# Performance work log

Measured on AMD Instinct MI355X. Metric: run time of the kernel, lower is better.

Reference implementation:

```python
import jax, jax.numpy as jnp
import numpy as np

C = 256
CQK = C // 8  # query/key projection dim


def setup_inputs() -> dict:
    key = jax.random.key(0)
    ks = jax.random.split(key, 8)
    B, H, W = 4, 64, 64
    x = jax.random.normal(ks[0], (B, C, H, W), dtype=jnp.float32)
    # 1x1 Conv1d == per-position linear: weight [out, in], bias [out]
    Wq = jax.random.normal(ks[1], (CQK, C), dtype=jnp.float32) * (1.0 / np.sqrt(C))
    bq = jax.random.normal(ks[2], (CQK,), dtype=jnp.float32) * 0.01
    Wk = jax.random.normal(ks[3], (CQK, C), dtype=jnp.float32) * (1.0 / np.sqrt(C))
    bk = jax.random.normal(ks[4], (CQK,), dtype=jnp.float32) * 0.01
    Wv = jax.random.normal(ks[5], (C, C), dtype=jnp.float32) * (1.0 / np.sqrt(C))
    bv = jax.random.normal(ks[6], (C,), dtype=jnp.float32) * 0.01
    gamma = jax.random.normal(ks[7], (1,), dtype=jnp.float32) * 0.1
    return {"x": x, "Wq": Wq, "bq": bq, "Wk": Wk, "bk": bk,
            "Wv": Wv, "bv": bv, "gamma": gamma}


def reference(x, Wq, bq, Wk, bk, Wv, bv, gamma):
    B, Cc, H, W = x.shape
    xf = x.reshape(B, Cc, H * W)                      # [B, C, N]
    q = jnp.einsum('oc,bcn->bon', Wq, xf) + bq[:, None]   # [B, C/8, N]
    k = jnp.einsum('oc,bcn->bon', Wk, xf) + bk[:, None]   # [B, C/8, N]
    v = jnp.einsum('oc,bcn->bon', Wv, xf) + bv[:, None]   # [B, C,   N]
    # energy = q^T k  (unscaled, SAGAN-style)
    energy = jnp.einsum('bon,bom->bnm', q, k)              # [B, N, N]
    attn = jax.nn.softmax(energy, axis=-1)                 # rows over key dim
    # out = value @ attention^T
    out = jnp.einsum('bcm,bnm->bcn', v, attn)              # [B, C, N]
    out = out.reshape(B, Cc, H, W)
    return gamma * out + x
```

## Files before the change

kernel.cpp:

```cpp
#include <hip/hip_runtime.h>
#include <math.h>
#include <stdint.h>

#define N_POS 4096
#define C_DIM 256
#define CQK_D 32
#define NSPLIT 3

typedef __attribute__((ext_vector_type(8))) short bf16x8;
typedef __attribute__((ext_vector_type(4))) float f32x4;
typedef __attribute__((ext_vector_type(4))) uint32_t u32x4;

__device__ inline uint16_t f2bf(float f){
  uint32_t u = __float_as_uint(f);
  return (uint16_t)((u + 0x7FFFu + ((u>>16)&1u)) >> 16);
}
__device__ inline uint32_t pk2bf(float a, float b){
  return (uint32_t)f2bf(a) | ((uint32_t)f2bf(b)<<16);
}
__device__ inline float bf2f_lo(uint32_t d){ return __uint_as_float(d << 16); }
__device__ inline float bf2f_hi(uint32_t d){ return __uint_as_float(d & 0xFFFF0000u); }

__global__ __launch_bounds__(256) void prep(
    const float* __restrict__ x,
    const float* __restrict__ Wq, const float* __restrict__ bq,
    const float* __restrict__ Wk, const float* __restrict__ bk,
    const float* __restrict__ Wv, const float* __restrict__ bv,
    ushort* __restrict__ xT_bf, ushort* __restrict__ W_bf, float* __restrict__ bias_f)
{
    const int tid = threadIdx.x;
    if (blockIdx.x == 64) {
        const int sub = blockIdx.z * 4 + blockIdx.y;
        const int e0 = sub * 5120;
        for (int e = e0 + tid; e < e0 + 5120; e += 256) {
            const int o = e >> 8, c = e & 255;
            float w;
            if (o < 32)       w = Wq[o*C_DIM + c];
            else if (o < 64)  w = Wk[(o-32)*C_DIM + c];
            else              w = Wv[(o-64)*C_DIM + c];
            W_bf[e] = f2bf(w);
        }
        if (sub == 0) {
            for (int i = tid; i < 320; i += 256)
                bias_f[i] = (i < 32) ? bq[i] : (i < 64) ? bk[i-32] : bv[i-64];
        }
        return;
    }
    __shared__ float t[64][65];
    const int jj = tid & 63;
    const int ig = tid >> 6;
    const int n0 = blockIdx.x * 64;
    const int c0 = blockIdx.y * 64;
    const int b  = blockIdx.z;
    #pragma unroll
    for (int ii = 0; ii < 16; ++ii) {
        const int cl = ii*4 + ig;
        t[cl][jj] = x[((size_t)(b*C_DIM) + c0 + cl)*N_POS + n0 + jj];
    }
    __syncthreads();
    #pragma unroll
    for (int ii = 0; ii < 8; ++ii) {
        const int flat = ii*256 + tid;
        const int nl = flat >> 5;
        const int cp = flat & 31;
        const uint32_t d = pk2bf(t[2*cp][nl], t[2*cp+1][nl]);
        *reinterpret_cast<uint32_t*>(xT_bf + ((size_t)(b*N_POS) + n0 + nl)*C_DIM + c0 + 2*cp) = d;
    }
}

__global__ __launch_bounds__(256, 2) void qkv_gemm(
    const ushort* __restrict__ xT_bf, const ushort* __restrict__ W_bf,
    const float* __restrict__ bias_f,
    ushort* __restrict__ q_bf, ushort* __restrict__ k_bf, ushort* __restrict__ v_bf)
{
    __shared__ ushort xs[64*C_DIM];
    const int tid  = threadIdx.x;
    const int wv   = tid >> 6;
    const int lane = tid & 63;
    const int g    = lane >> 4;
    const int q    = lane & 15;
    const int b    = blockIdx.y;
    const int n0   = blockIdx.x * 64;

    {
        const char* xTb = (const char*)(xT_bf + ((size_t)(b*N_POS) + n0)*C_DIM);
        const int n_l    = (tid*16) >> 9;
        const int inner  = (tid & 31) << 4;
        #pragma unroll
        for (int s = 0; s < 8; ++s) {
            const int n = s*8 + n_l;
            const int src_inner = inner ^ ((n & 7) << 4);
            __builtin_amdgcn_global_load_lds(
                (const __attribute__((address_space(1))) uint32_t*)(xTb + (size_t)n*512 + src_inner),
                (__attribute__((address_space(3))) uint32_t*)((char*)xs + s*4096 + wv*1024),
                16, 0, 0);
        }
    }
    __syncthreads();

    f32x4 zero4 = {0.f,0.f,0.f,0.f};
    f32x4 acc[20];
    #pragma unroll
    for (int i = 0; i < 20; ++i) acc[i] = zero4;

    const char* xrow = (const char*)xs + (wv*16 + q)*512;
    const int sw = (q & 7) << 4;

    #pragma unroll
    for (int kk = 0; kk < 8; ++kk) {
        const bf16x8 xf = *reinterpret_cast<const bf16x8*>(xrow + ((kk*64 + g*16) ^ sw));
        const ushort* wrow = W_bf + q*C_DIM + kk*32 + g*8;
        #pragma unroll
        for (int ot = 0; ot < 20; ++ot) {
            const bf16x8 wf = *reinterpret_cast<const bf16x8*>(wrow + ot*16*C_DIM);
            acc[ot] = __builtin_amdgcn_mfma_f32_16x16x32_bf16(wf, xf, acc[ot], 0, 0, 0);
        }
    }

    const int n = n0 + wv*16 + q;
    #pragma unroll
    for (int ot = 0; ot < 4; ++ot) {
        const int ob = ot*16 + 4*g;
        const float4 bi = *reinterpret_cast<const float4*>(bias_f + ob);
        const uint32_t u0 = pk2bf(acc[ot][0] + bi.x, acc[ot][1] + bi.y);
        const uint32_t u1 = pk2bf(acc[ot][2] + bi.z, acc[ot][3] + bi.w);
        ushort* dst = (ot < 2 ? q_bf : k_bf) + ((size_t)(b*N_POS) + n)*CQK_D + (ob & 31);
        uint2 u; u.x = u0; u.y = u1;
        *reinterpret_cast<uint2*>(dst) = u;
    }
    ushort* vB = v_bf + (size_t)(b*C_DIM)*N_POS + n;
    #pragma unroll
    for (int ot = 4; ot < 20; ++ot) {
        const int ob = ot*16 + 4*g;
        const float4 bi = *reinterpret_cast<const float4*>(bias_f + ob);
        const int c = ob - 64;
        vB[(size_t)(c+0)*N_POS] = f2bf(acc[ot][0] + bi.x);
        vB[(size_t)(c+1)*N_POS] = f2bf(acc[ot][1] + bi.y);
        vB[(size_t)(c+2)*N_POS] = f2bf(acc[ot][2] + bi.z);
        vB[(size_t)(c+3)*N_POS] = f2bf(acc[ot][3] + bi.w);
    }
}

__global__ __launch_bounds__(256, 3) void flash_mfma(
    const ushort* __restrict__ q_bf, const ushort* __restrict__ k_bf,
    const ushort* __restrict__ v_bf, ushort* __restrict__ o_part,
    float2* __restrict__ ml)
{
    __shared__ ushort vt[C_DIM*64];
    __shared__ ushort pt[4*16*64];
    __shared__ float  f_s[64];

    const int tid  = threadIdx.x;
    const int wv   = tid >> 6;
    const int lane = tid & 63;
    const int g    = lane >> 4;
    const int q    = lane & 15;
    const int half = blockIdx.y;
    const int b    = blockIdx.z;
    const int n0   = blockIdx.x * 64;
    const int qrow = n0 + wv*16 + q;
    const int mt0  = (half == 0) ? 0 : 22 + (half-1)*21;
    const int mt1  = mt0 + ((half == 0) ? 22 : 21);

    const ushort* qb = q_bf + (size_t)b*N_POS*CQK_D;
    const ushort* kb = k_bf + (size_t)b*N_POS*CQK_D;
    const ushort* vb = v_bf + (size_t)b*C_DIM*N_POS;

    const bf16x8 qfrag = *reinterpret_cast<const bf16x8*>(qb + (size_t)qrow*CQK_D + g*8);

    f32x4 zero4 = {0.f, 0.f, 0.f, 0.f};
    f32x4 acc[4][4];
    #pragma unroll
    for (int i = 0; i < 4; ++i)
        #pragma unroll
        for (int j = 0; j < 4; ++j) acc[i][j] = zero4;
    float m = -INFINITY, l = 0.f;

    const int st_hi = lane >> 3, st_lo = lane & 7;
    const ushort* vsrc0 = vb + (size_t)(wv*64 + st_hi)*N_POS + st_lo*8;
    char* vdst0 = (char*)vt + (wv*64 + st_hi)*128 + (((st_lo ^ st_hi) & 7) << 4);
    char* ptw   = (char*)pt + wv*2048;
    const int swq = (q & 7) << 4;

    auto loadK = [&](int mtx, bf16x8* kf) {
        const int mm = mtx * 64;
        #pragma unroll
        for (int t = 0; t < 4; ++t)
            kf[t] = *reinterpret_cast<const bf16x8*>(kb + (size_t)(mm + t*16 + q)*CQK_D + g*8);
    };

    auto chunk = [&](int mtx, bf16x8* kfc, bf16x8* kfn, int pfmt) {
        const int m0 = mtx * 64;
        __syncthreads();

        u32x4 vreg[8];
        #pragma unroll
        for (int s = 0; s < 8; ++s)
            vreg[s] = *reinterpret_cast<const u32x4*>(vsrc0 + (size_t)s*8*N_POS + m0);

        f32x4 sv[4];
        #pragma unroll
        for (int t = 0; t < 4; ++t)
            sv[t] = __builtin_amdgcn_mfma_f32_16x16x32_bf16(kfc[t], qfrag, zero4, 0, 0, 0);

        float pmax = sv[0][0];
        #pragma unroll
        for (int t = 0; t < 4; ++t)
            #pragma unroll
            for (int r = 0; r < 4; ++r) pmax = fmaxf(pmax, sv[t][r]);
        pmax = fmaxf(pmax, __shfl_xor(pmax, 16));
        pmax = fmaxf(pmax, __shfl_xor(pmax, 32));
        float f = 1.f;
        if (__any(pmax > m + 8.f)) {
            const float mn = fmaxf(m, pmax);
            f = __expf(m - mn);
            l *= f;
            m = mn;
        }
        if (g == 0) f_s[wv*16 + q] = f;

        uint32_t pk[8];
        float psum = 0.f;
        #pragma unroll
        for (int t = 0; t < 4; ++t) {
            const float p0 = __expf(sv[t][0]-m), p1 = __expf(sv[t][1]-m);
            const float p2 = __expf(sv[t][2]-m), p3 = __expf(sv[t][3]-m);
            psum += (p0+p1)+(p2+p3);
            pk[2*t]   = pk2bf(p0, p1);
            pk[2*t+1] = pk2bf(p2, p3);
        }
        psum += __shfl_xor(psum, 16);
        psum += __shfl_xor(psum, 32);
        l += psum;

        loadK(pfmt, kfn);

        #pragma unroll
        for (int t = 0; t < 4; ++t) {
            const int a = q*128 + ((t*32 + g*8) ^ swq);
            *reinterpret_cast<uint32_t*>(ptw + a)     = pk[2*t];
            *reinterpret_cast<uint32_t*>(ptw + a + 4) = pk[2*t+1];
        }
        #pragma unroll
        for (int s = 0; s < 8; ++s)
            *reinterpret_cast<u32x4*>(vdst0 + s*1024) = vreg[s];

        __syncthreads();

        float f4[4];
        #pragma unroll
        for (int qt = 0; qt < 4; ++qt) f4[qt] = f_s[qt*16 + q];
        const bool anyr = (f4[0]!=1.f) | (f4[1]!=1.f) | (f4[2]!=1.f) | (f4[3]!=1.f);
        if (__any(anyr)) {
            #pragma unroll
            for (int ct = 0; ct < 4; ++ct)
                #pragma unroll
                for (int qt = 0; qt < 4; ++qt) acc[ct][qt] *= f4[qt];
        }

        #pragma unroll
        for (int mm = 0; mm < 2; ++mm) {
            bf16x8 vf[4];
            #pragma unroll
            for (int ct = 0; ct < 4; ++ct)
                vf[ct] = *reinterpret_cast<const bf16x8*>(
                    (char*)vt + (wv*64 + ct*16 + q)*128 + ((mm*64 + g*16) ^ swq));
            #pragma unroll
            for (int qt = 0; qt < 4; ++qt) {
                const bf16x8 pb = *reinterpret_cast<const bf16x8*>(
                    (char*)pt + qt*2048 + q*128 + ((mm*64 + g*16) ^ swq));
                #pragma unroll
                for (int ct = 0; ct < 4; ++ct)
                    acc[ct][qt] = __builtin_amdgcn_mfma_f32_16x16x32_bf16(vf[ct], pb, acc[ct][qt], 0, 0, 0);
            }
        }
    };

    bf16x8 kfA[4], kfB[4];
    loadK(mt0, kfA);
    int mt = mt0;
    for (; mt + 1 < mt1; mt += 2) {
        chunk(mt,   kfA, kfB, mt + 1);
        chunk(mt+1, kfB, kfA, (mt + 2 < mt1) ? mt + 2 : mt1 - 1);
    }
    if (mt < mt1) chunk(mt, kfA, kfB, mt);

    if (g == 0) {
        float2 v; v.x = m; v.y = l;
        ml[(size_t)((half*4 + b)*N_POS) + qrow] = v;
    }

    __syncthreads();
    if (g == 0) f_s[wv*16 + q] = l;
    __syncthreads();
    float invl[4];
    #pragma unroll
    for (int qt = 0; qt < 4; ++qt) invl[qt] = 1.f / f_s[qt*16 + q];

    char* obase = (char*)o_part + ((size_t)((half*4 + b)*N_POS) + n0)*512;
    #pragma unroll
    for (int qt = 0; qt < 4; ++qt) {
        char* orow = obase + (size_t)(qt*16 + q)*512 + (wv*64 + 4*g)*2;
        #pragma unroll
        for (int ct = 0; ct < 4; ++ct) {
            const uint32_t u0 = pk2bf(acc[ct][qt][0]*invl[qt], acc[ct][qt][1]*invl[qt]);
            const uint32_t u1 = pk2bf(acc[ct][qt][2]*invl[qt], acc[ct][qt][3]*invl[qt]);
            uint2 u; u.x = u0; u.y = u1;
            *reinterpret_cast<uint2*>(orow + ct*32) = u;
        }
    }
}

__global__ __launch_bounds__(256) void out_combine(
    const ushort* __restrict__ o_part, const float2* __restrict__ ml,
    const float* __restrict__ x, const float* __restrict__ gamma,
    float* __restrict__ out)
{
    __shared__ float t[64][65];
    __shared__ float w0s[64], w1s[64], w2s[64];
    const int tid = threadIdx.x;
    const int jj = tid & 63;
    const int ig = tid >> 6;
    const int nt = blockIdx.x;
    const int ct = blockIdx.y;
    const int b  = blockIdx.z;
    const int n0 = nt*64, c0 = ct*64;
    const float gm = gamma[0];

    if (tid < 64) {
        const float2 a0 = ml[(size_t)((0*4 + b)*N_POS) + n0 + tid];
        const float2 a1 = ml[(size_t)((1*4 + b)*N_POS) + n0 + tid];
        const float2 a2 = ml[(size_t)((2*4 + b)*N_POS) + n0 + tid];
        const float mm = fmaxf(a0.x, fmaxf(a1.x, a2.x));
        const float e0 = __expf(a0.x - mm) * a0.y;
        const float e1 = __expf(a1.x - mm) * a1.y;
        const float e2 = __expf(a2.x - mm) * a2.y;
        const float inv = 1.f / (e0 + e1 + e2);
        w0s[tid] = e0 * inv;
        w1s[tid] = e1 * inv;
        w2s[tid] = e2 * inv;
    }
    __syncthreads();

    #pragma unroll
    for (int ii = 0; ii < 8; ++ii) {
        const int flat = ii*256 + tid;
        const int nl = flat >> 5;
        const int cp = flat & 31;
        const size_t off = ((size_t)(b*N_POS) + n0 + nl)*C_DIM + c0 + 2*cp;
        const uint32_t d0 = *reinterpret_cast<const uint32_t*>(o_part + off);
        const uint32_t d1 = *reinterpret_cast<const uint32_t*>(o_part + (size_t)4*N_POS*C_DIM + off);
        const uint32_t d2 = *reinterpret_cast<const uint32_t*>(o_part + (size_t)8*N_POS*C_DIM + off);
        const float w0 = w0s[nl], w1 = w1s[nl], w2 = w2s[nl];
        t[nl][2*cp]   = w0*bf2f_lo(d0) + w1*bf2f_lo(d1) + w2*bf2f_lo(d2);
        t[nl][2*cp+1] = w0*bf2f_hi(d0) + w1*bf2f_hi(d1) + w2*bf2f_hi(d2);
    }
    __syncthreads();
    #pragma unroll
    for (int ii = 0; ii < 16; ++ii) {
        const int cl = ii*4 + ig;
        const size_t idx = ((size_t)(b*C_DIM) + c0 + cl)*N_POS + n0 + jj;
        out[idx] = gm * t[jj][cl] + x[idx];
    }
}

extern "C" void kernel_launch(void* const* d_in, const int* in_sizes, int n_in,
                              void* d_out, int out_size, void* d_ws, size_t ws_size,
                              hipStream_t stream)
{
    const float* x     = (const float*)d_in[0];
    const float* Wq    = (const float*)d_in[1];
    const float* bq    = (const float*)d_in[2];
    const float* Wk    = (const float*)d_in[3];
    const float* bk    = (const float*)d_in[4];
    const float* Wv    = (const float*)d_in[5];
    const float* bv    = (const float*)d_in[6];
    const float* gamma = (const float*)d_in[7];

    ushort* o_part = (ushort*)d_ws;
    ushort* xT_bf  = (ushort*)d_ws;
    float2* ml     = (float2*)(o_part + (size_t)NSPLIT*4*N_POS*C_DIM);
    ushort* q_bf   = (ushort*)(ml + (size_t)NSPLIT*4*N_POS);
    ushort* k_bf   = q_bf + (size_t)4*N_POS*CQK_D;
    ushort* v_bf   = k_bf + (size_t)4*N_POS*CQK_D;
    ushort* W_bf   = v_bf + (size_t)4*C_DIM*N_POS;
    float*  bias_f = (float*)(W_bf + 320*C_DIM);
    float* out = (float*)d_out;

    prep<<<dim3(65,4,4), 256, 0, stream>>>(x, Wq, bq, Wk, bk, Wv, bv, xT_bf, W_bf, bias_f);
    qkv_gemm<<<dim3(64,4), 256, 0, stream>>>(xT_bf, W_bf, bias_f, q_bf, k_bf, v_bf);
    flash_mfma<<<dim3(64,NSPLIT,4), 256, 0, stream>>>(q_bf, k_bf, v_bf, o_part, ml);
    out_combine<<<dim3(64,4,4), 256, 0, stream>>>(o_part, ml, x, gamma, out);
}
```

Baseline: 115.2 us.

## Load V fragments directly from global in flash kernel and split QKV GEMM outputs

In the attention kernel, V tiles no longer go through LDS. Each wave loads its V MFMA fragments straight from global memory into registers, and the P tile is double-buffered in LDS so one barrier per chunk can be dropped. The QKV projection GEMM is split across two blocks along the output-channel dimension, which doubles the grid and halves the accumulators per thread for better occupancy and parallelism. The risks are less coalesced V global loads, since each lane now reads 16-byte pieces from separate rows, and the x tile being loaded into LDS twice.

After: 128.1 us. 11.2% more time.

```diff
diff --git a/kernel.cpp b/kernel.cpp
--- a/kernel.cpp
+++ b/kernel.cpp
@@ -79,7 +79,8 @@
     const int lane = tid & 63;
     const int g    = lane >> 4;
     const int q    = lane & 15;
-    const int b    = blockIdx.y;
+    const int y    = blockIdx.y;
+    const int b    = blockIdx.z;
     const int n0   = blockIdx.x * 64;
 
     {
@@ -99,9 +100,9 @@
     __syncthreads();
 
     f32x4 zero4 = {0.f,0.f,0.f,0.f};
-    f32x4 acc[20];
-    #pragma unroll
-    for (int i = 0; i < 20; ++i) acc[i] = zero4;
+    f32x4 acc[10];
+    #pragma unroll
+    for (int i = 0; i < 10; ++i) acc[i] = zero4;
 
     const char* xrow = (const char*)xs + (wv*16 + q)*512;
     const int sw = (q & 7) << 4;
@@ -109,35 +110,34 @@
     #pragma unroll
     for (int kk = 0; kk < 8; ++kk) {
         const bf16x8 xf = *reinterpret_cast<const bf16x8*>(xrow + ((kk*64 + g*16) ^ sw));
-        const ushort* wrow = W_bf + q*C_DIM + kk*32 + g*8;
-        #pragma unroll
-        for (int ot = 0; ot < 20; ++ot) {
-            const bf16x8 wf = *reinterpret_cast<const bf16x8*>(wrow + ot*16*C_DIM);
-            acc[ot] = __builtin_amdgcn_mfma_f32_16x16x32_bf16(wf, xf, acc[ot], 0, 0, 0);
+        const ushort* wrow = W_bf + (y*10*16 + q)*C_DIM + kk*32 + g*8;
+        #pragma unroll
+        for (int i = 0; i < 10; ++i) {
+            const bf16x8 wf = *reinterpret_cast<const bf16x8*>(wrow + i*16*C_DIM);
+            acc[i] = __builtin_amdgcn_mfma_f32_16x16x32_bf16(wf, xf, acc[i], 0, 0, 0);
         }
     }
 
     const int n = n0 + wv*16 + q;
     #pragma unroll
-    for (int ot = 0; ot < 4; ++ot) {
-        const int ob = ot*16 + 4*g;
+    for (int i = 0; i < 10; ++i) {
+        const int got = y*10 + i;
+        const int ob  = got*16 + 4*g;
         const float4 bi = *reinterpret_cast<const float4*>(bias_f + ob);
-        const uint32_t u0 = pk2bf(acc[ot][0] + bi.x, acc[ot][1] + bi.y);
-        const uint32_t u1 = pk2bf(acc[ot][2] + bi.z, acc[ot][3] + bi.w);
-        ushort* dst = (ot < 2 ? q_bf : k_bf) + ((size_t)(b*N_POS) + n)*CQK_D + (ob & 31);
-        uint2 u; u.x = u0; u.y = u1;
-        *reinterpret_cast<uint2*>(dst) = u;
-    }
-    ushort* vB = v_bf + (size_t)(b*C_DIM)*N_POS + n;
-    #pragma unroll
-    for (int ot = 4; ot < 20; ++ot) {
-        const int ob = ot*16 + 4*g;
-        const float4 bi = *reinterpret_cast<const float4*>(bias_f + ob);
-        const int c = ob - 64;
-        vB[(size_t)(c+0)*N_POS] = f2bf(acc[ot][0] + bi.x);
-        vB[(size_t)(c+1)*N_POS] = f2bf(acc[ot][1] + bi.y);
-        vB[(size_t)(c+2)*N_POS] = f2bf(acc[ot][2] + bi.z);
-        vB[(size_t)(c+3)*N_POS] = f2bf(acc[ot][3] + bi.w);
+        if (got < 4) {
+            const uint32_t u0 = pk2bf(acc[i][0] + bi.x, acc[i][1] + bi.y);
+            const uint32_t u1 = pk2bf(acc[i][2] + bi.z, acc[i][3] + bi.w);
+            ushort* dst = (got < 2 ? q_bf : k_bf) + ((size_t)(b*N_POS) + n)*CQK_D + (ob & 31);
+            uint2 u; u.x = u0; u.y = u1;
+            *reinterpret_cast<uint2*>(dst) = u;
+        } else {
+            const int c = ob - 64;
+            ushort* vB = v_bf + (size_t)(b*C_DIM)*N_POS + n;
+            vB[(size_t)(c+0)*N_POS] = f2bf(acc[i][0] + bi.x);
+            vB[(size_t)(c+1)*N_POS] = f2bf(acc[i][1] + bi.y);
+            vB[(size_t)(c+2)*N_POS] = f2bf(acc[i][2] + bi.z);
+            vB[(size_t)(c+3)*N_POS] = f2bf(acc[i][3] + bi.w);
+        }
     }
 }
 
@@ -146,9 +146,9 @@
     const ushort* __restrict__ v_bf, ushort* __restrict__ o_part,
     float2* __restrict__ ml)
 {
-    __shared__ ushort vt[C_DIM*64];
-    __shared__ ushort pt[4*16*64];
-    __shared__ float  f_s[64];
+    __shared__ ushort pt[2][4*16*64];
+    __shared__ float  f_s[2][64];
+    __shared__ float  l_s[64];
 
     const int tid  = threadIdx.x;
     const int wv   = tid >> 6;
@@ -176,11 +176,8 @@
         for (int j = 0; j < 4; ++j) acc[i][j] = zero4;
     float m = -INFINITY, l = 0.f;
 
-    const int st_hi = lane >> 3, st_lo = lane & 7;
-    const ushort* vsrc0 = vb + (size_t)(wv*64 + st_hi)*N_POS + st_lo*8;
-    char* vdst0 = (char*)vt + (wv*64 + st_hi)*128 + (((st_lo ^ st_hi) & 7) << 4);
-    char* ptw   = (char*)pt + wv*2048;
     const int swq = (q & 7) << 4;
+    const ushort* vbl = vb + (size_t)(wv*64 + q)*N_POS;
 
     auto loadK = [&](int mtx, bf16x8* kf) {
         const int mm = mtx * 64;
@@ -191,12 +188,16 @@
 
     auto chunk = [&](int mtx, bf16x8* kfc, bf16x8* kfn, int pfmt) {
         const int m0 = mtx * 64;
-        __syncthreads();
-
-        u32x4 vreg[8];
-        #pragma unroll
-        for (int s = 0; s < 8; ++s)
-            vreg[s] = *reinterpret_cast<const u32x4*>(vsrc0 + (size_t)s*8*N_POS + m0);
+        const int buf = mtx & 1;
+        char* ptw = (char*)pt[buf] + wv*2048;
+
+        bf16x8 vf[8];
+        #pragma unroll
+        for (int ct = 0; ct < 4; ++ct)
+            #pragma unroll
+            for (int mm = 0; mm < 2; ++mm)
+                vf[ct*2+mm] = *reinterpret_cast<const bf16x8*>(
+                    vbl + (size_t)(ct*16)*N_POS + m0 + mm*32 + g*8);
 
         f32x4 sv[4];
         #pragma unroll
@@ -217,7 +218,7 @@
             l *= f;
             m = mn;
         }
-        if (g == 0) f_s[wv*16 + q] = f;
+        if (g == 0) f_s[buf][wv*16 + q] = f;
 
         uint32_t pk[8];
         float psum = 0.f;
@@ -233,23 +234,20 @@
         psum += __shfl_xor(psum, 32);
         l += psum;
 
-        loadK(pfmt, kfn);
-
         #pragma unroll
         for (int t = 0; t < 4; ++t) {
             const int a = q*128 + ((t*32 + g*8) ^ swq);
             *reinterpret_cast<uint32_t*>(ptw + a)     = pk[2*t];
             *reinterpret_cast<uint32_t*>(ptw + a + 4) = pk[2*t+1];
         }
-        #pragma unroll
-        for (int s = 0; s < 8; ++s)
-            *reinterpret_cast<u32x4*>(vdst0 + s*1024) = vreg[s];
+
+        loadK(pfmt, kfn);
 
         __syncthreads();
 
         float f4[4];
         #pragma unroll
-        for (int qt = 0; qt < 4; ++qt) f4[qt] = f_s[qt*16 + q];
+        for (int qt = 0; qt < 4; ++qt) f4[qt] = f_s[buf][qt*16 + q];
         const bool anyr = (f4[0]!=1.f) | (f4[1]!=1.f) | (f4[2]!=1.f) | (f4[3]!=1.f);
         if (__any(anyr)) {
             #pragma unroll
@@ -260,18 +258,13 @@
 
         #pragma unroll
         for (int mm = 0; mm < 2; ++mm) {
-            bf16x8 vf[4];
-            #pragma unroll
-            for (int ct = 0; ct < 4; ++ct)
-                vf[ct] = *reinterpret_cast<const bf16x8*>(
-                    (char*)vt + (wv*64 + ct*16 + q)*128 + ((mm*64 + g*16) ^ swq));
             #pragma unroll
             for (int qt = 0; qt < 4; ++qt) {
                 const bf16x8 pb = *reinterpret_cast<const bf16x8*>(
-                    (char*)pt + qt*2048 + q*128 + ((mm*64 + g*16) ^ swq));
+                    (char*)pt[buf] + qt*2048 + q*128 + ((mm*64 + g*16) ^ swq));
                 #pragma unroll
                 for (int ct = 0; ct < 4; ++ct)
-                    acc[ct][qt] = __builtin_amdgcn_mfma_f32_16x16x32_bf16(vf[ct], pb, acc[ct][qt], 0, 0, 0);
+                    acc[ct][qt] = __builtin_amdgcn_mfma_f32_16x16x32_bf16(vf[ct*2+mm], pb, acc[ct][qt], 0, 0, 0);
             }
         }
     };
@@ -290,12 +283,11 @@
         ml[(size_t)((half*4 + b)*N_POS) + qrow] = v;
     }
 
-    __syncthreads();
-    if (g == 0) f_s[wv*16 + q] = l;
+    if (g == 0) l_s[wv*16 + q] = l;
     __syncthreads();
     float invl[4];
     #pragma unroll
-    for (int qt = 0; qt < 4; ++qt) invl[qt] = 1.f / f_s[qt*16 + q];
+    for (int qt = 0; qt < 4; ++qt) invl[qt] = 1.f / l_s[qt*16 + q];
 
     char* obase = (char*)o_part + ((size_t)((half*4 + b)*N_POS) + n0)*512;
     #pragma unroll
@@ -388,7 +380,7 @@
     float* out = (float*)d_out;
 
     prep<<<dim3(65,4,4), 256, 0, stream>>>(x, Wq, bq, Wk, bk, Wv, bv, xT_bf, W_bf, bias_f);
-    qkv_gemm<<<dim3(64,4), 256, 0, stream>>>(xT_bf, W_bf, bias_f, q_bf, k_bf, v_bf);
+    qkv_gemm<<<dim3(64,2,4), 256, 0, stream>>>(xT_bf, W_bf, bias_f, q_bf, k_bf, v_bf);
     flash_mfma<<<dim3(64,NSPLIT,4), 256, 0, stream>>>(q_bf, k_bf, v_bf, o_part, ml);
     out_combine<<<dim3(64,4,4), 256, 0, stream>>>(o_part, ml, x, gamma, out);
 }
```
